# Kernel optimization log

Hardware: AMD Instinct MI355X
Metric: run time of the kernel (lower is better)

## Reference

```python
import jax, jax.numpy as jnp
import numpy as np

D = 1024      # in_dim
HS = 64       # head_size
H = 16        # num_heads
B, S = 2, 2048


def setup_inputs() -> dict:
    key = jax.random.key(0)
    k1, k2, k3, k4, k5, k6 = jax.random.split(key, 6)
    scale = 1.0 / np.sqrt(D)
    x = jax.random.normal(k1, (B, S, D), dtype=jnp.float32)
    # Stacked per-head projection weights (torch Linear weight is [out,in];
    # random init so layout only needs to be consistent). query weight exists
    # in the torch module but is never used (source bug), so it is omitted.
    Wk = jax.random.normal(k2, (H, D, HS), dtype=jnp.float32) * scale
    Wv = jax.random.normal(k3, (H, D, HS), dtype=jnp.float32) * scale
    Wproj = jax.random.normal(k4, (H * HS, D), dtype=jnp.float32) * (1.0 / np.sqrt(H * HS))
    bproj = jax.random.normal(k5, (D,), dtype=jnp.float32) * 0.01
    return {"x": x, "Wk": Wk, "Wv": Wv, "Wproj": Wproj, "bproj": bproj}


def reference(x, Wk, Wv, Wproj, bproj):
    # Faithful to source: k = key(x); q = value(x); v = value(x)  (q == v, no softmax)
    k = jnp.einsum("bsd,hde->bhse", x, Wk)   # [B,H,S,HS]
    v = jnp.einsum("bsd,hde->bhse", x, Wv)   # [B,H,S,HS]
    q = v
    inv_sqrt = jnp.asarray(HS, x.dtype) ** -0.5
    wei = jnp.einsum("bhse,bhte->bhst", q, k) * inv_sqrt  # [B,H,S,S], unnormalized
    out = jnp.einsum("bhst,bhte->bhse", wei, v)            # [B,H,S,HS]
    # concat heads: [B,S,H*HS]
    out = jnp.transpose(out, (0, 2, 1, 3)).reshape(x.shape[0], x.shape[1], H * HS)
    return out @ Wproj + bproj  # [B,S,D]
```

## Files before the change

### kernel.cpp

```cpp
#include <hip/hip_runtime.h>

#define B_ 2
#define S_ 2048
#define D_ 1024
#define H_ 16
#define HS_ 64
#define HD_ 1024
#define BS_ (B_*S_)
#define BK_ 64
#define BKO_ 128
#define TP_ 136

typedef __attribute__((ext_vector_type(8))) short short8_t;
typedef __attribute__((ext_vector_type(4))) float float4_t;

__device__ inline unsigned short f32_to_bf16(float f) {
  unsigned int u = __float_as_uint(f);
  u += 0x7FFF + ((u >> 16) & 1);
  return (unsigned short)(u >> 16);
}

__device__ inline void async_copy16(const void* g, void* lds) {
  __builtin_amdgcn_global_load_lds(
      (const __attribute__((address_space(1))) void*)g,
      (__attribute__((address_space(3))) void*)lds, 16, 0, 0);
}


__global__ __launch_bounds__(256) void prep_kernel(
    const float* __restrict__ x, const float* __restrict__ Wk,
    const float* __restrict__ Wv, unsigned short* __restrict__ xb,
    unsigned short* __restrict__ Wkvt) {
  const int blk = blockIdx.x;
  const int tid = threadIdx.x;
  __shared__ float lds[64][65];
  if (blk < 4096) {
    int idx = blk * 256 + tid;
    float4 v = ((const float4*)x)[idx];
    ushort4 o;
    o.x = f32_to_bf16(v.x); o.y = f32_to_bf16(v.y);
    o.z = f32_to_bf16(v.z); o.w = f32_to_bf16(v.w);
    ((ushort4*)xb)[idx] = o;
    return;
  }
  const int wblk = blk - 4096;
  const int h = wblk >> 4;
  const int d0 = (wblk & 15) * 64;
#pragma unroll
  for (int i = 0; i < 16; ++i) {
    int idx = tid + i * 256; int dd = idx >> 6, e = idx & 63;
    lds[e][dd] = Wk[((size_t)h * D_ + d0 + dd) * HS_ + e];
  }
  __syncthreads();
#pragma unroll
  for (int i = 0; i < 16; ++i) {
    int idx = tid + i * 256; int e = idx >> 6, dd = idx & 63;
    Wkvt[((size_t)h * 128 + e) * D_ + d0 + dd] = f32_to_bf16(lds[e][dd]);
  }
  __syncthreads();
#pragma unroll
  for (int i = 0; i < 16; ++i) {
    int idx = tid + i * 256; int dd = idx >> 6, e = idx & 63;
    lds[e][dd] = Wv[((size_t)h * D_ + d0 + dd) * HS_ + e];
  }
  __syncthreads();
#pragma unroll
  for (int i = 0; i < 16; ++i) {
    int idx = tid + i * 256; int e = idx >> 6, dd = idx & 63;
    Wkvt[((size_t)h * 128 + 64 + e) * D_ + d0 + dd] = f32_to_bf16(lds[e][dd]);
  }
}

__global__ __launch_bounds__(256) void kv_mfma_kernel(
    const unsigned short* __restrict__ xb,
    const unsigned short* __restrict__ Wkvt,
    unsigned short* __restrict__ Vb,
    float* __restrict__ Mpart) {
  const int blk = blockIdx.x;
  const int stile = blk & 31;
  const int h = blk >> 5;
  const int s0 = stile * 128;
  const int tid = threadIdx.x;
  const int lane = tid & 63;
  const int wid = tid >> 6;
  const int wm = wid & 1, wn = wid >> 1;
  const int quad = lane >> 4, l16 = lane & 15;
  const int srow8 = lane >> 3;
  const int csw = ((lane & 7) ^ srow8) * 8;
  const int xa = l16 & 7;

  __shared__ __align__(16) unsigned char smem[2 * 64 * TP_ * 2];
  unsigned short* As  = (unsigned short*)smem;
  unsigned short* Bs  = (unsigned short*)(smem + 128 * BK_ * 2);
  unsigned short* Ktl = (unsigned short*)smem;
  unsigned short* Vtl = (unsigned short*)(smem + 64 * TP_ * 2);

  float4_t acc[4][4];
  const float4_t fz = {0.f, 0.f, 0.f, 0.f};
#pragma unroll
  for (int i = 0; i < 4; ++i)
#pragma unroll
    for (int j = 0; j < 4; ++j) acc[i][j] = fz;

  for (int k0 = 0; k0 < D_; k0 += BK_) {
#pragma unroll
    for (int i = 0; i < 4; ++i) {
      int g = wid * 4 + i;
      int r = g * 8 + srow8;
      async_copy16(xb + (size_t)(s0 + r) * D_ + k0 + csw, As + g * 8 * BK_);
      async_copy16(Wkvt + ((size_t)h * 128 + r) * D_ + k0 + csw, Bs + g * 8 * BK_);
    }
    __syncthreads();
    short8_t a[4][2], b[4][2];
#pragma unroll
    for (int mi = 0; mi < 4; ++mi)
#pragma unroll
      for (int ks = 0; ks < 2; ++ks)
        a[mi][ks] = *(const short8_t*)(As + (wm * 64 + mi * 16 + l16) * BK_ +
                                       ((ks * 4 + quad) ^ xa) * 8);
#pragma unroll
    for (int ni = 0; ni < 4; ++ni)
#pragma unroll
      for (int ks = 0; ks < 2; ++ks)
        b[ni][ks] = *(const short8_t*)(Bs + (wn * 64 + ni * 16 + l16) * BK_ +
                                       ((ks * 4 + quad) ^ xa) * 8);
#pragma unroll
    for (int ks = 0; ks < 2; ++ks)
#pragma unroll
      for (int mi = 0; mi < 4; ++mi)
#pragma unroll
        for (int ni = 0; ni < 4; ++ni)
          acc[mi][ni] = __builtin_amdgcn_mfma_f32_16x16x32_bf16(
              a[mi][ks], b[ni][ks], acc[mi][ni], 0, 0, 0);
    __syncthreads();
  }

  {
    unsigned short* dstT = (wn == 0) ? Ktl : Vtl;
#pragma unroll
    for (int mi = 0; mi < 4; ++mi)
#pragma unroll
      for (int ni = 0; ni < 4; ++ni) {
        int f = ni * 16 + l16;
        int sm = wm * 64 + mi * 16 + quad * 4;
        ushort4 o;
        o.x = f32_to_bf16(acc[mi][ni][0]);
        o.y = f32_to_bf16(acc[mi][ni][1]);
        o.z = f32_to_bf16(acc[mi][ni][2]);
        o.w = f32_to_bf16(acc[mi][ni][3]);
        *(ushort4*)&dstT[f * TP_ + sm] = o;
      }
  }
  __syncthreads();

#pragma unroll
  for (int u = 0; u < 4; ++u) {
    int unit = tid + u * 256;
    int s = unit & 127;
    int ec = (unit >> 7) * 8;
    union { unsigned short u16[8]; uint4 v; } t;
#pragma unroll
    for (int e = 0; e < 8; ++e) t.u16[e] = Vtl[(ec + e) * TP_ + s];
    *(uint4*)&Vb[(size_t)(s0 + s) * HD_ + h * 64 + ec] = t.v;
  }

  {
    float4_t macc[4];
#pragma unroll
    for (int ni = 0; ni < 4; ++ni) macc[ni] = fz;
#pragma unroll
    for (int ss = 0; ss < 4; ++ss) {
      short8_t ka = *(const short8_t*)&Ktl[(wid * 16 + l16) * TP_ + ss * 32 + quad * 8];
#pragma unroll
      for (int ni = 0; ni < 4; ++ni) {
        short8_t vv = *(const short8_t*)&Vtl[(ni * 16 + l16) * TP_ + ss * 32 + quad * 8];
        macc[ni] = __builtin_amdgcn_mfma_f32_16x16x32_bf16(ka, vv, macc[ni], 0, 0, 0);
      }
    }
    float* mdst = Mpart + ((size_t)stile * H_ + h) * 4096;
#pragma unroll
    for (int ni = 0; ni < 4; ++ni) {
      int e = ni * 16 + l16;
#pragma unroll
      for (int r = 0; r < 4; ++r) {
        int f = wid * 16 + quad * 4 + r;
        mdst[f * 64 + e] = macc[ni][r];
      }
    }
  }
}

__global__ __launch_bounds__(256) void m_reduce_kernel(
    const float* __restrict__ Mpart, float* __restrict__ M) {
  const int gid = blockIdx.x * 256 + threadIdx.x;
  const int e0 = gid * 4;
  const int bh = e0 >> 12;
  const int idx = e0 & 4095;
  const int b = bh >> 4, h = bh & 15;
  float4 s = {0.f, 0.f, 0.f, 0.f};
#pragma unroll
  for (int p = 0; p < 16; ++p) {
    const float4 v =
        *(const float4*)&Mpart[(((size_t)(b * 16 + p)) * H_ + h) * 4096 + idx];
    s.x += v.x; s.y += v.y; s.z += v.z; s.w += v.w;
  }
  s.x *= 0.125f; s.y *= 0.125f; s.z *= 0.125f; s.w *= 0.125f;
  *(float4*)&M[(size_t)bh * 4096 + idx] = s;
}

__global__ __launch_bounds__(256) void p_kernel(
    const float* __restrict__ M, const float* __restrict__ Wproj,
    unsigned short* __restrict__ Pt) {
  const int blk = blockIdx.x;
  const int dtile = blk & 15;
  const int h = (blk >> 4) & 15;
  const int b = blk >> 8;
  const int d0 = dtile * 64;
  const int tid = threadIdx.x;
  const int tx = tid & 15, ty = tid >> 4;
  __shared__ float Ms[64][68];
  __shared__ float Ws[64][68];
  const size_t mbase = ((size_t)(b * H_ + h)) * HS_ * HS_;
#pragma unroll
  for (int i = 0; i < 16; ++i) {
    int idx = tid + i * 256;
    int f = idx >> 6, e = idx & 63;
    Ms[e][f] = M[mbase + idx];
    Ws[f][e] = Wproj[(size_t)(h * HS_ + f) * D_ + d0 + e];
  }
  __syncthreads();
  float acc[4][4] = {};
#pragma unroll
  for (int kk = 0; kk < 64; ++kk) {
    const float4 a4 = *(const float4*)&Ms[kk][ty * 4];
    const float4 b4 = *(const float4*)&Ws[kk][tx * 4];
    const float a[4] = {a4.x, a4.y, a4.z, a4.w};
    const float bb[4] = {b4.x, b4.y, b4.z, b4.w};
#pragma unroll
    for (int i = 0; i < 4; ++i)
#pragma unroll
      for (int j = 0; j < 4; ++j) acc[i][j] += a[i] * bb[j];
  }
  __syncthreads();
#pragma unroll
  for (int i = 0; i < 4; ++i)
#pragma unroll
    for (int j = 0; j < 4; ++j)
      Ms[tx * 4 + j][ty * 4 + i] = acc[i][j];
  __syncthreads();
  {
    int c = tid >> 2, ch = tid & 3;
    unsigned short* dst = Pt + ((size_t)(b * D_ + d0 + c)) * HD_ + h * 64 + ch * 16;
#pragma unroll
    for (int e = 0; e < 16; ++e) dst[e] = f32_to_bf16(Ms[c][ch * 16 + e]);
  }
}

__global__ __launch_bounds__(256) void out_mfma_kernel(
    const unsigned short* __restrict__ Vb,
    const unsigned short* __restrict__ Pt,
    const float* __restrict__ bproj,
    float* __restrict__ out) {
  const int blk = blockIdx.x;
  const int ntile = blk & 15;
  const int stile = blk >> 4;
  const int s0 = stile * 128;
  const int n0 = ntile * 64;
  const int b = s0 >> 11;
  const int tid = threadIdx.x;
  const int lane = tid & 63;
  const int wid = tid >> 6;
  const int wm = wid & 1, wn = wid >> 1;
  const int quad = lane >> 4, l16 = lane & 15;
  const int srow4 = lane >> 4;
  const int xa = l16 & 7;

  __shared__ __align__(16) unsigned short As[128 * BKO_];
  __shared__ __align__(16) unsigned short Bs[64 * BKO_];

  float4_t acc[4][2];
  const float4_t fz = {0.f, 0.f, 0.f, 0.f};
#pragma unroll
  for (int i = 0; i < 4; ++i)
#pragma unroll
    for (int j = 0; j < 2; ++j) acc[i][j] = fz;

  const unsigned short* Bpanel = Pt + (size_t)b * D_ * HD_;
  for (int k0 = 0; k0 < HD_; k0 += BKO_) {
#pragma unroll
    for (int i = 0; i < 8; ++i) {
      int g = wid * 8 + i;
      int r = g * 4 + srow4;
      int ch = (l16 ^ (r & 7)) * 8;
      async_copy16(Vb + (size_t)(s0 + r) * HD_ + k0 + ch, As + g * 4 * BKO_);
    }
#pragma unroll
    for (int i = 0; i < 4; ++i) {
      int g = wid * 4 + i;
      int r = g * 4 + srow4;
      int ch = (l16 ^ (r & 7)) * 8;
      async_copy16(Bpanel + (size_t)(n0 + r) * HD_ + k0 + ch, Bs + g * 4 * BKO_);
    }
    __syncthreads();
    short8_t a[4][4], bfr[2][4];
#pragma unroll
    for (int mi = 0; mi < 4; ++mi)
#pragma unroll
      for (int ks = 0; ks < 4; ++ks)
        a[mi][ks] = *(const short8_t*)(As + (wm * 64 + mi * 16 + l16) * BKO_ +
                                       ((ks * 4 + quad) ^ xa) * 8);
#pragma unroll
    for (int ni = 0; ni < 2; ++ni)
#pragma unroll
      for (int ks = 0; ks < 4; ++ks)
        bfr[ni][ks] = *(const short8_t*)(Bs + (wn * 32 + ni * 16 + l16) * BKO_ +
                                         ((ks * 4 + quad) ^ xa) * 8);
#pragma unroll
    for (int ks = 0; ks < 4; ++ks)
#pragma unroll
      for (int mi = 0; mi < 4; ++mi)
#pragma unroll
        for (int ni = 0; ni < 2; ++ni)
          acc[mi][ni] = __builtin_amdgcn_mfma_f32_16x16x32_bf16(
              a[mi][ks], bfr[ni][ks], acc[mi][ni], 0, 0, 0);
    __syncthreads();
  }
#pragma unroll
  for (int ni = 0; ni < 2; ++ni) {
    int col = n0 + wn * 32 + ni * 16 + l16;
    float bias = bproj[col];
#pragma unroll
    for (int mi = 0; mi < 4; ++mi) {
      int rowb = s0 + wm * 64 + mi * 16 + quad * 4;
#pragma unroll
      for (int r = 0; r < 4; ++r)
        out[(size_t)(rowb + r) * D_ + col] = acc[mi][ni][r] + bias;
    }
  }
}

extern "C" void kernel_launch(void* const* d_in, const int* in_sizes, int n_in,
                              void* d_out, int out_size, void* d_ws, size_t ws_size,
                              hipStream_t stream) {
  const float* x = (const float*)d_in[0];
  const float* Wk = (const float*)d_in[1];
  const float* Wv = (const float*)d_in[2];
  const float* Wproj = (const float*)d_in[3];
  const float* bproj = (const float*)d_in[4];
  float* out = (float*)d_out;

  char* ws = (char*)d_ws;
  unsigned short* xb = (unsigned short*)ws;
  unsigned short* Wkvt = xb + (size_t)BS_ * D_;
  unsigned short* Vb = Wkvt + (size_t)H_ * 128 * D_;
  float* Mpart = (float*)(Vb + (size_t)BS_ * HD_);
  float* M = Mpart + (size_t)32 * H_ * 4096;
  unsigned short* Pt = (unsigned short*)(M + (size_t)B_ * H_ * 4096);

  prep_kernel<<<dim3(4096 + H_ * (D_ / 64)), dim3(256), 0, stream>>>(x, Wk, Wv, xb, Wkvt);
  kv_mfma_kernel<<<dim3(32 * H_), dim3(256), 0, stream>>>(xb, Wkvt, Vb, Mpart);
  m_reduce_kernel<<<dim3(128), dim3(256), 0, stream>>>(Mpart, M);
  p_kernel<<<dim3(B_ * H_ * (D_ / 64)), dim3(256), 0, stream>>>(M, Wproj, Pt);
  out_mfma_kernel<<<dim3(32 * 16), dim3(256), 0, stream>>>(Vb, Pt, bproj, out);
}
```

Measured before the change: 133.6 us.

## Process two heads per KV block and widen output tiles with 512-thread blocks

The K/V projection kernel now runs 512 threads per block and covers two heads per block, so each x tile loaded into shared memory is reused for 256 weight columns rather than 128. The output GEMM also uses 512-thread blocks with 128-wide N tiles, so each V tile is reused across more output columns. Both changes halve the grid size, to 256 blocks, which cuts redundant global loads but may leave fewer blocks per CU and less latency hiding. Shared memory use per block also grows.

```diff
diff --git a/kernel.cpp b/kernel.cpp
--- a/kernel.cpp
+++ b/kernel.cpp
@@ -71,14 +71,14 @@
   }
 }
 
-__global__ __launch_bounds__(256) void kv_mfma_kernel(
+__global__ __launch_bounds__(512) void kv_mfma_kernel(
     const unsigned short* __restrict__ xb,
     const unsigned short* __restrict__ Wkvt,
     unsigned short* __restrict__ Vb,
     float* __restrict__ Mpart) {
   const int blk = blockIdx.x;
   const int stile = blk & 31;
-  const int h = blk >> 5;
+  const int hp = blk >> 5;
   const int s0 = stile * 128;
   const int tid = threadIdx.x;
   const int lane = tid & 63;
@@ -89,11 +89,9 @@
   const int csw = ((lane & 7) ^ srow8) * 8;
   const int xa = l16 & 7;
 
-  __shared__ __align__(16) unsigned char smem[2 * 64 * TP_ * 2];
-  unsigned short* As  = (unsigned short*)smem;
-  unsigned short* Bs  = (unsigned short*)(smem + 128 * BK_ * 2);
-  unsigned short* Ktl = (unsigned short*)smem;
-  unsigned short* Vtl = (unsigned short*)(smem + 64 * TP_ * 2);
+  __shared__ __align__(16) unsigned char smem[4 * 64 * TP_ * 2];
+  unsigned short* As = (unsigned short*)smem;
+  unsigned short* Bs = (unsigned short*)(smem + 128 * BK_ * 2);
 
   float4_t acc[4][4];
   const float4_t fz = {0.f, 0.f, 0.f, 0.f};
@@ -102,13 +100,19 @@
 #pragma unroll
     for (int j = 0; j < 4; ++j) acc[i][j] = fz;
 
+  const unsigned short* Bpanel = Wkvt + (size_t)hp * 256 * D_;
   for (int k0 = 0; k0 < D_; k0 += BK_) {
+#pragma unroll
+    for (int i = 0; i < 2; ++i) {
+      int g = wid * 2 + i;
+      int r = g * 8 + srow8;
+      async_copy16(xb + (size_t)(s0 + r) * D_ + k0 + csw, As + g * 8 * BK_);
+    }
 #pragma unroll
     for (int i = 0; i < 4; ++i) {
       int g = wid * 4 + i;
       int r = g * 8 + srow8;
-      async_copy16(xb + (size_t)(s0 + r) * D_ + k0 + csw, As + g * 8 * BK_);
-      async_copy16(Wkvt + ((size_t)h * 128 + r) * D_ + k0 + csw, Bs + g * 8 * BK_);
+      async_copy16(Bpanel + (size_t)r * D_ + k0 + csw, Bs + g * 8 * BK_);
     }
     __syncthreads();
     short8_t a[4][2], b[4][2];
@@ -136,7 +140,7 @@
   }
 
   {
-    unsigned short* dstT = (wn == 0) ? Ktl : Vtl;
+    unsigned short* dstT = (unsigned short*)(smem + (size_t)wn * 64 * TP_ * 2);
 #pragma unroll
     for (int mi = 0; mi < 4; ++mi)
 #pragma unroll
@@ -155,35 +159,44 @@
 
 #pragma unroll
   for (int u = 0; u < 4; ++u) {
-    int unit = tid + u * 256;
+    int unit = tid + u * 512;
     int s = unit & 127;
-    int ec = (unit >> 7) * 8;
+    int ec = unit >> 7;
+    int hd = ec >> 3;
+    const unsigned short* vt =
+        (const unsigned short*)(smem + (size_t)(hd * 2 + 1) * 64 * TP_ * 2);
     union { unsigned short u16[8]; uint4 v; } t;
 #pragma unroll
-    for (int e = 0; e < 8; ++e) t.u16[e] = Vtl[(ec + e) * TP_ + s];
-    *(uint4*)&Vb[(size_t)(s0 + s) * HD_ + h * 64 + ec] = t.v;
+    for (int e = 0; e < 8; ++e) t.u16[e] = vt[((ec & 7) * 8 + e) * TP_ + s];
+    *(uint4*)&Vb[(size_t)(s0 + s) * HD_ + hp * 128 + hd * 64 + (ec & 7) * 8] = t.v;
   }
 
   {
+    const int hd = wid >> 2;
+    const int fw = (wid & 3) * 16;
+    const unsigned short* Ktl =
+        (const unsigned short*)(smem + (size_t)(hd * 2) * 64 * TP_ * 2);
+    const unsigned short* Vtl =
+        (const unsigned short*)(smem + (size_t)(hd * 2 + 1) * 64 * TP_ * 2);
     float4_t macc[4];
 #pragma unroll
     for (int ni = 0; ni < 4; ++ni) macc[ni] = fz;
 #pragma unroll
     for (int ss = 0; ss < 4; ++ss) {
-      short8_t ka = *(const short8_t*)&Ktl[(wid * 16 + l16) * TP_ + ss * 32 + quad * 8];
+      short8_t ka = *(const short8_t*)&Ktl[(fw + l16) * TP_ + ss * 32 + quad * 8];
 #pragma unroll
       for (int ni = 0; ni < 4; ++ni) {
         short8_t vv = *(const short8_t*)&Vtl[(ni * 16 + l16) * TP_ + ss * 32 + quad * 8];
         macc[ni] = __builtin_amdgcn_mfma_f32_16x16x32_bf16(ka, vv, macc[ni], 0, 0, 0);
       }
     }
-    float* mdst = Mpart + ((size_t)stile * H_ + h) * 4096;
+    float* mdst = Mpart + ((size_t)stile * H_ + hp * 2 + hd) * 4096;
 #pragma unroll
     for (int ni = 0; ni < 4; ++ni) {
       int e = ni * 16 + l16;
 #pragma unroll
       for (int r = 0; r < 4; ++r) {
-        int f = wid * 16 + quad * 4 + r;
+        int f = fw + quad * 4 + r;
         mdst[f * 64 + e] = macc[ni][r];
       }
     }
@@ -256,16 +269,16 @@
   }
 }
 
-__global__ __launch_bounds__(256) void out_mfma_kernel(
+__global__ __launch_bounds__(512) void out_mfma_kernel(
     const unsigned short* __restrict__ Vb,
     const unsigned short* __restrict__ Pt,
     const float* __restrict__ bproj,
     float* __restrict__ out) {
   const int blk = blockIdx.x;
-  const int ntile = blk & 15;
-  const int stile = blk >> 4;
+  const int ntile = blk & 7;
+  const int stile = blk >> 3;
   const int s0 = stile * 128;
-  const int n0 = ntile * 64;
+  const int n0 = ntile * 128;
   const int b = s0 >> 11;
   const int tid = threadIdx.x;
   const int lane = tid & 63;
@@ -276,7 +289,7 @@
   const int xa = l16 & 7;
 
   __shared__ __align__(16) unsigned short As[128 * BKO_];
-  __shared__ __align__(16) unsigned short Bs[64 * BKO_];
+  __shared__ __align__(16) unsigned short Bs[128 * BKO_];
 
   float4_t acc[4][2];
   const float4_t fz = {0.f, 0.f, 0.f, 0.f};
@@ -287,18 +300,18 @@
 
   const unsigned short* Bpanel = Pt + (size_t)b * D_ * HD_;
   for (int k0 = 0; k0 < HD_; k0 += BKO_) {
-#pragma unroll
-    for (int i = 0; i < 8; ++i) {
-      int g = wid * 8 + i;
-      int r = g * 4 + srow4;
-      int ch = (l16 ^ (r & 7)) * 8;
-      async_copy16(Vb + (size_t)(s0 + r) * HD_ + k0 + ch, As + g * 4 * BKO_);
-    }
 #pragma unroll
     for (int i = 0; i < 4; ++i) {
       int g = wid * 4 + i;
       int r = g * 4 + srow4;
-      int ch = (l16 ^ (r & 7)) * 8;
+      int ch = ((lane & 15) ^ (r & 7)) * 8;
+      async_copy16(Vb + (size_t)(s0 + r) * HD_ + k0 + ch, As + g * 4 * BKO_);
+    }
+#pragma unroll
+    for (int i = 0; i < 4; ++i) {
+      int g = wid * 4 + i;
+      int r = g * 4 + srow4;
+      int ch = ((lane & 15) ^ (r & 7)) * 8;
       async_copy16(Bpanel + (size_t)(n0 + r) * HD_ + k0 + ch, Bs + g * 4 * BKO_);
     }
     __syncthreads();
@@ -358,8 +371,8 @@
   unsigned short* Pt = (unsigned short*)(M + (size_t)B_ * H_ * 4096);
 
   prep_kernel<<<dim3(4096 + H_ * (D_ / 64)), dim3(256), 0, stream>>>(x, Wk, Wv, xb, Wkvt);
-  kv_mfma_kernel<<<dim3(32 * H_), dim3(256), 0, stream>>>(xb, Wkvt, Vb, Mpart);
+  kv_mfma_kernel<<<dim3(32 * 8), dim3(512), 0, stream>>>(xb, Wkvt, Vb, Mpart);
   m_reduce_kernel<<<dim3(128), dim3(256), 0, stream>>>(Mpart, M);
   p_kernel<<<dim3(B_ * H_ * (D_ / 64)), dim3(256), 0, stream>>>(M, Wproj, Pt);
-  out_mfma_kernel<<<dim3(32 * 16), dim3(256), 0, stream>>>(Vb, Pt, bproj, out);
-}
+  out_mfma_kernel<<<dim3(32 * 8), dim3(512), 0, stream>>>(Vb, Pt, bproj, out);
+}
```

New measurement: 140.7 us. 1.05x slower.
